# Optimization experiments

Hardware: AMD Instinct MI355X
Metric: run time of the kernel (lower is better)

## Reference

```python
import jax, jax.numpy as jnp
import numpy as np

B, T, C, H = 4, 2048, 768, 12
D = C // H  # head dim = 64
EPS = 1e-5


def setup_inputs() -> dict:
    key = jax.random.key(0)
    ks = jax.random.split(key, 12)
    s = lambda fan_in: 1.0 / np.sqrt(fan_in)
    return {
        "x": jax.random.normal(ks[0], (B, T, C), dtype=jnp.float32),
        "ln1_g": jnp.ones((C,), jnp.float32),
        "ln1_b": jnp.zeros((C,), jnp.float32),
        "w_attn": jax.random.normal(ks[1], (C, 3 * C), jnp.float32) * s(C),
        "b_attn": jnp.zeros((3 * C,), jnp.float32),
        "w_aproj": jax.random.normal(ks[2], (C, C), jnp.float32) * s(C),
        "b_aproj": jnp.zeros((C,), jnp.float32),
        "ln2_g": jnp.ones((C,), jnp.float32),
        "ln2_b": jnp.zeros((C,), jnp.float32),
        "w_fc": jax.random.normal(ks[3], (C, 4 * C), jnp.float32) * s(C),
        "b_fc": jnp.zeros((4 * C,), jnp.float32),
        "w_mproj": jax.random.normal(ks[4], (4 * C, C), jnp.float32) * s(4 * C),
        "b_mproj": jnp.zeros((C,), jnp.float32),
    }


def _layernorm(x, g, b):
    mu = jnp.mean(x, axis=-1, keepdims=True)
    var = jnp.mean(jnp.square(x - mu), axis=-1, keepdims=True)
    return (x - mu) * jax.lax.rsqrt(var + EPS) * g + b


def _attention(h, w_attn, b_attn, w_aproj, b_aproj):
    qkv = h @ w_attn + b_attn                          # [B,T,3C]
    q, k, v = jnp.split(qkv, 3, axis=-1)
    q = q.reshape(B, T, H, D)
    k = k.reshape(B, T, H, D)
    v = v.reshape(B, T, H, D)
    att = jnp.einsum("bqhd,bkhd->bhqk", q, k) * (1.0 / np.sqrt(D))
    causal = jnp.tril(jnp.ones((T, T), bool))
    att = jnp.where(causal, att, -jnp.inf)
    att = jax.nn.softmax(att, axis=-1)
    y = jnp.einsum("bhqk,bkhd->bqhd", att, v).reshape(B, T, C)
    return y @ w_aproj + b_aproj


def reference(x, ln1_g, ln1_b, w_attn, b_attn, w_aproj, b_aproj,
              ln2_g, ln2_b, w_fc, b_fc, w_mproj, b_mproj):
    x = x + _attention(_layernorm(x, ln1_g, ln1_b), w_attn, b_attn, w_aproj, b_aproj)
    h = _layernorm(x, ln2_g, ln2_b)
    h = jax.nn.gelu(h @ w_fc + b_fc, approximate=True)  # tanh approximation, matches F.gelu(approximate='tanh')
    x = x + (h @ w_mproj + b_mproj)
    return x
```

## Files before the change

### kernel.cpp

```cpp
#include <hip/hip_runtime.h>


typedef unsigned short ushortT;
typedef unsigned int uintT;
typedef __attribute__((ext_vector_type(8))) __bf16 bf16x8;
typedef __attribute__((ext_vector_type(4))) float f32x4;

#define MFMA16(a, b, c) __builtin_amdgcn_mfma_f32_16x16x32_bf16(a, b, c, 0, 0, 0)

__device__ inline float b2f(ushortT u) {
  return __uint_as_float(((uintT)u) << 16);
}
__device__ inline ushortT f2b(float f) {
  uintT x = __float_as_uint(f);
  uintT r = x + 0x7fffu + ((x >> 16) & 1u);
  return (ushortT)(r >> 16);
}
__device__ inline uintT pack_bf2(float a, float b) {
  return __builtin_amdgcn_perm(__float_as_uint(b), __float_as_uint(a),
                               0x07060302u);
}

__device__ inline float fast_exp2(float x) {
#if __has_builtin(__builtin_amdgcn_exp2f)
  return __builtin_amdgcn_exp2f(x);
#else
  return exp2f(x);
#endif
}

__device__ inline float gelu_tanh(float v) {
  float t = 0.7978845608028654f * (v + 0.044715f * v * v * v);
  return v / (1.0f + __expf(-2.0f * t));
}

__device__ __forceinline__ void glds16(const ushortT* g, ushortT* l) {
  __builtin_amdgcn_global_load_lds(
      (const __attribute__((address_space(1))) unsigned int*)(const void*)g,
      (__attribute__((address_space(3))) unsigned int*)(void*)l, 16, 0, 0);
}

struct VecArgs {
  const void* src[8];
  int n[8];
  int dstoff[8];
};

__global__ __launch_bounds__(256) void prep_kernel(
    const void* __restrict__ w_attn, const void* __restrict__ w_aproj,
    const void* __restrict__ w_fc, const void* __restrict__ w_mproj,
    VecArgs va, ushortT* __restrict__ wT0, ushortT* __restrict__ wT1,
    ushortT* __restrict__ wT2, ushortT* __restrict__ wT3,
    ushortT* __restrict__ pv, int* __restrict__ flag,
    const void* __restrict__ x, const void* __restrict__ ln1g,
    const void* __restrict__ ln1b, ushortT* __restrict__ h1) {
  __shared__ int sfl;
  __shared__ ushortT tile[32][33];
  __shared__ float as_[4], aq_[4];
  int tid = threadIdx.x;
  {
    int crazy = 0;
    if (tid < 64) {
      uintT e = (((const ushortT*)w_fc)[2 * (tid * 64)] >> 7) & 0xFF;
      crazy = (e >= 150) ? 1 : 0;
    }
    unsigned long long m = __ballot(crazy != 0);
    if (tid == 0) sfl = (m != 0ull) ? 1 : 0;
    __syncthreads();
  }
  int fl = sfl;
  int b = (int)blockIdx.x;
  if (b == 0 && tid == 0) *flag = fl;

  const int T0 = 1728;
  const int T1 = T0 + 576;
  const int T2 = T1 + 2304;
  const int T3 = T2 + 2304;
  const int T4 = T3 + 39;

  if (b >= T4) {
    int row = b - T4;
    size_t base = (size_t)row * 768;
    const float* xf = (const float*)x;
    const ushortT* xb = (const ushortT*)x;
    float v0 = fl ? xf[base + tid]       : b2f(xb[base + tid]);
    float v1 = fl ? xf[base + tid + 256] : b2f(xb[base + tid + 256]);
    float v2 = fl ? xf[base + tid + 512] : b2f(xb[base + tid + 512]);
    float s = v0 + v1 + v2;
    float q = v0 * v0 + v1 * v1 + v2 * v2;
#pragma unroll
    for (int off = 32; off; off >>= 1) {
      s += __shfl_xor(s, off);
      q += __shfl_xor(q, off);
    }
    if ((tid & 63) == 0) { as_[tid >> 6] = s; aq_[tid >> 6] = q; }
    __syncthreads();
    s = as_[0] + as_[1] + as_[2] + as_[3];
    q = aq_[0] + aq_[1] + aq_[2] + aq_[3];
    float mu = s * (1.0f / 768.0f);
    float var = q * (1.0f / 768.0f) - mu * mu;
    float rs = rsqrtf(var + 1e-5f);
    const float* gf = (const float*)ln1g;
    const ushortT* gb_ = (const ushortT*)ln1g;
    const float* bf = (const float*)ln1b;
    const ushortT* bb_ = (const ushortT*)ln1b;
    ushortT* orow = h1 + base;
#pragma unroll
    for (int jj = 0; jj < 3; ++jj) {
      int c = tid + jj * 256;
      float gv = fl ? gf[c] : b2f(gb_[c]);
      float bv = fl ? bf[c] : b2f(bb_[c]);
      float vv = (jj == 0) ? v0 : (jj == 1) ? v1 : v2;
      orow[c] = f2b((vv - mu) * rs * gv + bv);
    }
    return;
  }

  const void* in = nullptr;
  ushortT* out = nullptr;
  int K = 0, N = 0, gx = 0, t = 0;
  if (b < T0)      { in = w_attn;  out = wT0; K = 768;  N = 2304; gx = 72; t = b; }
  else if (b < T1) { in = w_aproj; out = wT1; K = 768;  N = 768;  gx = 24; t = b - T0; }
  else if (b < T2) { in = w_fc;    out = wT2; K = 768;  N = 3072; gx = 96; t = b - T1; }
  else if (b < T3) { in = w_mproj; out = wT3; K = 3072; N = 768;  gx = 24; t = b - T2; }
  else {
    int c = b - T3;
    int v = 0;
    for (;;) {
      int nch = (va.n[v] + 255) >> 8;
      if (c < nch) break;
      c -= nch; ++v;
    }
    int i = c * 256 + tid;
    if (i < va.n[v]) {
      float xx = fl ? ((const float*)va.src[v])[i]
                    : b2f(((const ushortT*)va.src[v])[i]);
      pv[va.dstoff[v] + i] = f2b(xx);
    }
    return;
  }

  int n0 = (t % gx) * 32, k0 = (t / gx) * 32;
  int xx = tid & 31, y0 = tid >> 5;
#pragma unroll
  for (int i = y0; i < 32; i += 8) {
    size_t idx = (size_t)(k0 + i) * N + n0 + xx;
    tile[i][xx] = fl ? f2b(((const float*)in)[idx]) : ((const ushortT*)in)[idx];
  }
  __syncthreads();
#pragma unroll
  for (int i = y0; i < 32; i += 8)
    out[(size_t)(n0 + i) * K + k0 + xx] = tile[xx][i];
}

template <int MODE>
__global__ __launch_bounds__(256) void ln_kernel(
    const void* __restrict__ xin, const ushortT* __restrict__ g,
    const ushortT* __restrict__ bb, ushortT* __restrict__ out,
    const int* __restrict__ flag) {
  const int C = 768;
  bool f32;
  if constexpr (MODE == 1) f32 = true; else f32 = (*flag != 0);
  size_t base = (size_t)blockIdx.x * C;
  int tid = threadIdx.x;
  const float* xf = (const float*)xin;
  const ushortT* xb = (const ushortT*)xin;
  float v0 = f32 ? xf[base + tid]       : b2f(xb[base + tid]);
  float v1 = f32 ? xf[base + tid + 256] : b2f(xb[base + tid + 256]);
  float v2 = f32 ? xf[base + tid + 512] : b2f(xb[base + tid + 512]);
  float s = v0 + v1 + v2;
  float q = v0 * v0 + v1 * v1 + v2 * v2;
#pragma unroll
  for (int off = 32; off; off >>= 1) {
    s += __shfl_xor(s, off);
    q += __shfl_xor(q, off);
  }
  __shared__ float as_[4], aq_[4];
  if ((tid & 63) == 0) { as_[tid >> 6] = s; aq_[tid >> 6] = q; }
  __syncthreads();
  s = as_[0] + as_[1] + as_[2] + as_[3];
  q = aq_[0] + aq_[1] + aq_[2] + aq_[3];
  float mu = s * (1.0f / 768.0f);
  float var = q * (1.0f / 768.0f) - mu * mu;
  float rs = rsqrtf(var + 1e-5f);
  ushortT* orow = out + base;
  orow[tid]       = f2b((v0 - mu) * rs * b2f(g[tid])       + b2f(bb[tid]));
  orow[tid + 256] = f2b((v1 - mu) * rs * b2f(g[tid + 256]) + b2f(bb[tid + 256]));
  orow[tid + 512] = f2b((v2 - mu) * rs * b2f(g[tid + 512]) + b2f(bb[tid + 512]));
}

template <int EPI, int BN>
__global__ __launch_bounds__(256, 2) void gemm_8p(
    const ushortT* __restrict__ A, const ushortT* __restrict__ Bt,
    const ushortT* __restrict__ bias, const void* __restrict__ res,
    void* __restrict__ out, int N, int K, int lda, int nbm, int nbn,
    const int* __restrict__ flag) {
  constexpr int MI = (BN == 256) ? 8 : 4;
  constexpr int NI = 4;
  __shared__ ushortT As3[3][128 * 32];
  __shared__ ushortT Bs3[3][BN * 32];
  int fl = (EPI == 2 || EPI == 3) ? *flag : 0;
  int tid = threadIdx.x;
  int lane = tid & 63, wave = tid >> 6;
  int quad = lane >> 4, n = lane & 15;
  int wm, wn;
  if constexpr (BN == 256) { wm = 0; wn = wave * 64; }
  else { wm = (wave >> 1) * 64; wn = (wave & 1) * 64; }
  int l = blockIdx.x;
  int xcd = l & 7, j = l >> 3;
  int m0 = (xcd * (nbm >> 3) + j / nbn) * 128;
  int n0 = (j % nbn) * BN;

  int trow = tid >> 2;
  int tc = (((tid & 3) ^ ((trow >> 1) & 3)) << 3);
  const ushortT* ga = A + (size_t)(m0 + trow) * lda + tc;
  const ushortT* gb = Bt + (size_t)(n0 + trow) * lda + tc;

  const int cs = (quad ^ ((n >> 1) & 3)) << 3;

  int kt = K >> 5;
  f32x4 acc[MI][NI] = {};

  auto stage = [&](int tt, int slot) {
    int k0 = tt << 5;
    ushortT* la = &As3[slot][0] + wave * 512;
    ushortT* lb = &Bs3[slot][0] + wave * 512;
    glds16(ga + k0, la);
    glds16(ga + (size_t)64 * lda + k0, la + 2048);
    glds16(gb + k0, lb);
    glds16(gb + (size_t)64 * lda + k0, lb + 2048);
    if constexpr (BN == 256) {
      glds16(gb + (size_t)128 * lda + k0, lb + 4096);
      glds16(gb + (size_t)192 * lda + k0, lb + 6144);
    }
  };

  stage(0, 0);
  stage(1, 1);
  if constexpr (BN == 256)
    asm volatile("s_waitcnt vmcnt(6)" ::: "memory");
  else
    asm volatile("s_waitcnt vmcnt(4)" ::: "memory");
  __builtin_amdgcn_s_barrier();

  int cur = 0;
  for (int t = 0; t < kt; ++t) {
    const ushortT* ca = &As3[cur][0];
    const ushortT* cb = &Bs3[cur][0];
    int nxt = cur + 2; if (nxt >= 3) nxt -= 3;
    bool pf = (t + 2) < kt;
    int pk0 = (t + 2) << 5;
    ushortT* la = &As3[nxt][0] + wave * 512;
    ushortT* lb = &Bs3[nxt][0] + wave * 512;

    bf16x8 af[4], bfr[NI];
#pragma unroll
    for (int i = 0; i < 4; ++i)
      af[i] = *(const bf16x8*)(ca + (wm + i * 16 + n) * 32 + cs);
#pragma unroll
    for (int i = 0; i < NI; ++i)
      bfr[i] = *(const bf16x8*)(cb + (wn + i * 16 + n) * 32 + cs);
    if (pf) {
      glds16(ga + pk0, la);
      glds16(ga + (size_t)64 * lda + pk0, la + 2048);
      glds16(gb + pk0, lb);
      if constexpr (BN == 128)
        glds16(gb + (size_t)64 * lda + pk0, lb + 2048);
    }
    __builtin_amdgcn_s_barrier();
    __builtin_amdgcn_s_setprio(1);
#pragma unroll
    for (int mi = 0; mi < 4; ++mi)
#pragma unroll
      for (int ni = 0; ni < NI; ++ni)
        acc[mi][ni] = MFMA16(af[mi], bfr[ni], acc[mi][ni]);
    __builtin_amdgcn_s_setprio(0);
    if constexpr (BN == 256) {
      __builtin_amdgcn_s_barrier();
#pragma unroll
      for (int i = 0; i < 4; ++i)
        af[i] = *(const bf16x8*)(ca + (64 + i * 16 + n) * 32 + cs);
      if (pf) {
        glds16(gb + (size_t)64 * lda + pk0, lb + 2048);
        glds16(gb + (size_t)128 * lda + pk0, lb + 4096);
        glds16(gb + (size_t)192 * lda + pk0, lb + 6144);
      }
      __builtin_amdgcn_s_barrier();
      __builtin_amdgcn_s_setprio(1);
#pragma unroll
      for (int mi = 0; mi < 4; ++mi)
#pragma unroll
        for (int ni = 0; ni < NI; ++ni)
          acc[4 + mi][ni] = MFMA16(af[mi], bfr[ni], acc[4 + mi][ni]);
      __builtin_amdgcn_s_setprio(0);
    }
    if (pf) {
      if constexpr (BN == 256)
        asm volatile("s_waitcnt vmcnt(6)" ::: "memory");
      else
        asm volatile("s_waitcnt vmcnt(4)" ::: "memory");
    } else {
      asm volatile("s_waitcnt vmcnt(0)" ::: "memory");
    }
    __builtin_amdgcn_s_barrier();

    cur = cur + 1; if (cur == 3) cur = 0;
  }

#pragma unroll
  for (int mi = 0; mi < MI; ++mi) {
#pragma unroll
    for (int ni = 0; ni < NI; ++ni) {
      int gc = n0 + wn + ni * 16 + n;
      float bv = b2f(bias[gc]);
      int gr0 = m0 + wm + mi * 16 + quad * 4;
      if constexpr (EPI == 5) {
        float v0 = acc[mi][ni][0] + bv;
        float v1 = acc[mi][ni][1] + bv;
        float v2 = acc[mi][ni][2] + bv;
        float v3 = acc[mi][ni][3] + bv;
        if (gc < 1536) {
          ushortT* o = (ushortT*)out;
          o[(size_t)(gr0 + 0) * N + gc] = f2b(v0);
          o[(size_t)(gr0 + 1) * N + gc] = f2b(v1);
          o[(size_t)(gr0 + 2) * N + gc] = f2b(v2);
          o[(size_t)(gr0 + 3) * N + gc] = f2b(v3);
        } else {
          int hh = (gc - 1536) >> 6, dd = (gc - 1536) & 63;
          int bb = gr0 >> 11, tin = gr0 & 2047;
          ushortT* vp = (ushortT*)res;
          uint2 o;
          o.x = (uintT)f2b(v0) | ((uintT)f2b(v1) << 16);
          o.y = (uintT)f2b(v2) | ((uintT)f2b(v3) << 16);
          *(uint2*)(vp + ((size_t)(bb * 12 + hh) * 64 + dd) * 2048 + tin) = o;
        }
      } else {
#pragma unroll
        for (int r = 0; r < 4; ++r) {
          size_t idx = (size_t)(gr0 + r) * N + gc;
          float v = acc[mi][ni][r] + bv;
          if constexpr (EPI == 1) {
            v = gelu_tanh(v);
            ((ushortT*)out)[idx] = f2b(v);
          } else if constexpr (EPI == 2) {
            v += fl ? ((const float*)res)[idx] : b2f(((const ushortT*)res)[idx]);
            ((float*)out)[idx] = v;
          } else if constexpr (EPI == 3) {
            v += ((const float*)res)[idx];
            if (fl) ((float*)out)[idx] = v;
            else    ((ushortT*)out)[idx] = f2b(v);
          } else {
            ((ushortT*)out)[idx] = f2b(v);
          }
        }
      }
    }
  }
}

__global__ __launch_bounds__(256) void attn_kernel(
    const ushortT* __restrict__ qkv, const ushortT* __restrict__ vt,
    ushortT* __restrict__ y) {
  const int T = 2048, C3 = 2304;
  constexpr int LDP = 72;
  __shared__ ushortT Ks[2][64 * 64];
  __shared__ ushortT Vs[2][64 * 64];
  __shared__ ushortT Ps[4 * 16 * LDP];
  int bh = blockIdx.y;
  int b = bh / 12, h = bh % 12;
  int pj = blockIdx.x;
  int tid = threadIdx.x;
  int lane = tid & 63, wave = tid >> 6;
  int quad = lane >> 4, n = lane & 15, n7 = n & 7;

  const ushortT* base = qkv + (size_t)b * T * C3;
  const ushortT* kbase = base + 768 + h * 64;
  const ushortT* vbase = vt + (size_t)bh * 64 * T;
  ushortT* myP = Ps + wave * 16 * LDP;

  const float QS = 0.18033688011112042f;
  const float MB = 20.0f;

  int qtA = pj, qtB = 31 - pj;
  int nA = qtA + 1, ntot = 33;

  int srow = lane >> 3, scol = lane & 7;
  const ushortT* kg =
      kbase + (size_t)(wave * 16 + srow) * C3 + ((scol ^ srow) << 3);
  const ushortT* vg =
      vbase + (size_t)(wave * 16 + srow) * T + ((scol ^ srow) << 3);

  const int c0 = (quad ^ n7) << 3;
  const int c1 = ((4 + quad) ^ n7) << 3;

  int qt = qtA;
  int qw = qt * 64 + wave * 16;
  bf16x8 aq[2];
  {
    const ushortT* qrow = base + (size_t)(qw + n) * C3 + h * 64 + quad * 8;
#pragma unroll
    for (int dh = 0; dh < 2; ++dh) {
      union { ushortT u[8]; bf16x8 v; } tmp;
#pragma unroll
      for (int j = 0; j < 8; ++j) tmp.u[j] = f2b(b2f(qrow[dh * 32 + j]) * QS);
      aq[dh] = tmp.v;
    }
  }
  f32x4 Ot[4] = {};
  float l_ = 0.f;

  auto stage = [&](int kt_, int buf) {
    int kof = kt_ << 6;
    ushortT* lk = &Ks[buf][0] + wave * 1024;
    ushortT* lv = &Vs[buf][0] + wave * 1024;
    glds16(kg + (size_t)kof * C3, lk);
    glds16(kg + (size_t)(kof + 8) * C3, lk + 512);
    glds16(vg + kof, lv);
    glds16(vg + (size_t)8 * T + kof, lv + 512);
  };

  stage(0, 0);
  __syncthreads();

  int cur = 0;
  for (int t = 0; t < ntot; ++t) {
    int kt = (t < nA) ? t : t - nA;
    if (t + 1 < ntot) {
      int ktn = (t + 1 < nA) ? t + 1 : t + 1 - nA;
      stage(ktn, cur ^ 1);
    }
    const ushortT* ks = &Ks[cur][0];
    const ushortT* vs = &Vs[cur][0];

    f32x4 St[4];
#pragma unroll
    for (int g = 0; g < 4; ++g) {
      bf16x8 ka0 = *(const bf16x8*)(ks + (g * 16 + n) * 64 + c0);
      bf16x8 ka1 = *(const bf16x8*)(ks + (g * 16 + n) * 64 + c1);
      f32x4 z = {};
      z = MFMA16(ka0, aq[0], z);
      St[g] = MFMA16(ka1, aq[1], z);
    }
    if (kt == qt) {
      int lim = wave * 16 + n;
#pragma unroll
      for (int g = 0; g < 4; ++g)
#pragma unroll
        for (int r = 0; r < 4; ++r)
          if (g * 16 + quad * 4 + r > lim) St[g][r] = -1e30f;
    }
    float ls = 0.f;
#pragma unroll
    for (int g = 0; g < 4; ++g) {
      float p0 = fast_exp2(St[g][0] - MB);
      float p1 = fast_exp2(St[g][1] - MB);
      float p2 = fast_exp2(St[g][2] - MB);
      float p3 = fast_exp2(St[g][3] - MB);
      ls += (p0 + p1) + (p2 + p3);
      uint2 pk;
      pk.x = pack_bf2(p0, p1);
      pk.y = pack_bf2(p2, p3);
      *(uint2*)(myP + n * LDP + g * 16 + quad * 4) = pk;
    }
    ls += __shfl_xor(ls, 16);
    ls += __shfl_xor(ls, 32);
    l_ += ls;

    bf16x8 pb0 = *(const bf16x8*)(myP + n * LDP + quad * 8);
    bf16x8 pb1 = *(const bf16x8*)(myP + n * LDP + 32 + quad * 8);
#pragma unroll
    for (int dt = 0; dt < 4; ++dt) {
      bf16x8 va0 = *(const bf16x8*)(vs + (dt * 16 + n) * 64 + c0);
      bf16x8 va1 = *(const bf16x8*)(vs + (dt * 16 + n) * 64 + c1);
      Ot[dt] = MFMA16(va0, pb0, Ot[dt]);
      Ot[dt] = MFMA16(va1, pb1, Ot[dt]);
    }

    if (kt == qt) {
      float inv = 1.0f / l_;
      int qg = qw + n;
#pragma unroll
      for (int dt = 0; dt < 4; ++dt) {
        uint2 o;
        o.x = pack_bf2(Ot[dt][0] * inv, Ot[dt][1] * inv);
        o.y = pack_bf2(Ot[dt][2] * inv, Ot[dt][3] * inv);
        *(uint2*)(y + (size_t)(b * T + qg) * 768 + h * 64 + dt * 16 +
                  quad * 4) = o;
      }
      if (t + 1 < ntot) {
        qt = qtB;
        qw = qt * 64 + wave * 16;
        const ushortT* qrow =
            base + (size_t)(qw + n) * C3 + h * 64 + quad * 8;
#pragma unroll
        for (int dh = 0; dh < 2; ++dh) {
          union { ushortT u[8]; bf16x8 v; } tmp;
#pragma unroll
          for (int j = 0; j < 8; ++j)
            tmp.u[j] = f2b(b2f(qrow[dh * 32 + j]) * QS);
          aq[dh] = tmp.v;
        }
#pragma unroll
        for (int dt = 0; dt < 4; ++dt)
#pragma unroll
          for (int r = 0; r < 4; ++r) Ot[dt][r] = 0.f;
        l_ = 0.f;
      }
    }
    __syncthreads();
    cur ^= 1;
  }
}

extern "C" void kernel_launch(void* const* d_in, const int* in_sizes, int n_in,
                              void* d_out, int out_size, void* d_ws,
                              size_t ws_size, hipStream_t stream) {
  (void)in_sizes; (void)n_in; (void)out_size; (void)ws_size;
  const void* x       = d_in[0];
  const void* w_attn  = d_in[3];
  const void* w_aproj = d_in[5];
  const void* w_fc    = d_in[9];
  const void* w_mproj = d_in[11];

  char* ws = (char*)d_ws;
  ushortT* h1  = (ushortT*)(ws);
  ushortT* qkv = (ushortT*)(ws + 12582912);
  ushortT* yb  = (ushortT*)(ws + 50331648);
  float*   x1  = (float*)(ws + 62914560);
  ushortT* fcg = (ushortT*)(ws + 88080384);
  ushortT* wT0 = (ushortT*)(ws + 138412032);
  ushortT* wT1 = (ushortT*)(ws + 141950976);
  ushortT* wT2 = (ushortT*)(ws + 143130624);
  ushortT* wT3 = (ushortT*)(ws + 147849216);
  ushortT* pv  = (ushortT*)(ws + 152567808);
  int*     flag = (int*)(ws + 152600576);
  ushortT* vt  = fcg;
  ushortT* h2  = yb;

  const int O_LN1G = 0, O_LN1B = 768, O_BATT = 1536, O_BAPR = 3840,
            O_LN2G = 4608, O_LN2B = 5376, O_BFC = 6144, O_BMPR = 9216;

  VecArgs va;
  va.src[0] = d_in[1];  va.n[0] = 768;  va.dstoff[0] = O_LN1G;
  va.src[1] = d_in[2];  va.n[1] = 768;  va.dstoff[1] = O_LN1B;
  va.src[2] = d_in[4];  va.n[2] = 2304; va.dstoff[2] = O_BATT;
  va.src[3] = d_in[6];  va.n[3] = 768;  va.dstoff[3] = O_BAPR;
  va.src[4] = d_in[7];  va.n[4] = 768;  va.dstoff[4] = O_LN2G;
  va.src[5] = d_in[8];  va.n[5] = 768;  va.dstoff[5] = O_LN2B;
  va.src[6] = d_in[10]; va.n[6] = 3072; va.dstoff[6] = O_BFC;
  va.src[7] = d_in[12]; va.n[7] = 768;  va.dstoff[7] = O_BMPR;

  prep_kernel<<<15143, 256, 0, stream>>>(
      w_attn, w_aproj, w_fc, w_mproj, va, wT0, wT1, wT2, wT3, pv, flag,
      x, d_in[1], d_in[2], h1);

  gemm_8p<5, 256><<<576, 256, 0, stream>>>(
      h1, wT0, pv + O_BATT, vt, qkv, 2304, 768, 768, 64, 9, flag);
  attn_kernel<<<dim3(16, 48), 256, 0, stream>>>(qkv, vt, yb);
  gemm_8p<2, 128><<<384, 256, 0, stream>>>(
      yb, wT1, pv + O_BAPR, x, x1, 768, 768, 768, 64, 6, flag);
  ln_kernel<1><<<8192, 256, 0, stream>>>(x1, pv + O_LN2G, pv + O_LN2B, h2, flag);
  gemm_8p<1, 256><<<768, 256, 0, stream>>>(
      h2, wT2, pv + O_BFC, nullptr, fcg, 3072, 768, 768, 64, 12, flag);
  gemm_8p<3, 128><<<384, 256, 0, stream>>>(
      fcg, wT3, pv + O_BMPR, x1, d_out, 768, 3072, 3072, 64, 6, flag);
}
```

Before: 402.0 us.

## Share K/V tile loads between paired query tiles in causal attention

The attention kernel used to walk the two paired query tiles one after the other, restaging K/V for the second tile. Now both tiles' queries stay in registers and a single pass over key tiles (32-pj of them) feeds both. Tile B uses every key tile and tile A only the first pj+1, which cuts K/V staging and barrier iterations from 33 to at most 32, and the shared tiles are loaded once. The cost is higher register pressure from two sets of Q, O and S accumulators, which may lower occupancy.

```diff
diff --git a/kernel.cpp b/kernel.cpp
--- a/kernel.cpp
+++ b/kernel.cpp
@@ -382,7 +382,7 @@
   const float MB = 20.0f;
 
   int qtA = pj, qtB = 31 - pj;
-  int nA = qtA + 1, ntot = 33;
+  int ntiles = 32 - pj;
 
   int srow = lane >> 3, scol = lane & 7;
   const ushortT* kg =
@@ -393,21 +393,26 @@
   const int c0 = (quad ^ n7) << 3;
   const int c1 = ((4 + quad) ^ n7) << 3;
 
-  int qt = qtA;
-  int qw = qt * 64 + wave * 16;
-  bf16x8 aq[2];
+  bf16x8 aqA[2], aqB[2];
   {
-    const ushortT* qrow = base + (size_t)(qw + n) * C3 + h * 64 + quad * 8;
+    const ushortT* qrA =
+        base + (size_t)(qtA * 64 + wave * 16 + n) * C3 + h * 64 + quad * 8;
+    const ushortT* qrB =
+        base + (size_t)(qtB * 64 + wave * 16 + n) * C3 + h * 64 + quad * 8;
 #pragma unroll
     for (int dh = 0; dh < 2; ++dh) {
-      union { ushortT u[8]; bf16x8 v; } tmp;
-#pragma unroll
-      for (int j = 0; j < 8; ++j) tmp.u[j] = f2b(b2f(qrow[dh * 32 + j]) * QS);
-      aq[dh] = tmp.v;
-    }
-  }
-  f32x4 Ot[4] = {};
-  float l_ = 0.f;
+      union { ushortT u[8]; bf16x8 v; } ta, tb;
+#pragma unroll
+      for (int j = 0; j < 8; ++j) {
+        ta.u[j] = f2b(b2f(qrA[dh * 32 + j]) * QS);
+        tb.u[j] = f2b(b2f(qrB[dh * 32 + j]) * QS);
+      }
+      aqA[dh] = ta.v;
+      aqB[dh] = tb.v;
+    }
+  }
+  f32x4 OtA[4] = {}, OtB[4] = {};
+  float lA = 0.f, lB = 0.f;
 
   auto stage = [&](int kt_, int buf) {
     int kof = kt_ << 6;
@@ -423,92 +428,138 @@
   __syncthreads();
 
   int cur = 0;
-  for (int t = 0; t < ntot; ++t) {
-    int kt = (t < nA) ? t : t - nA;
-    if (t + 1 < ntot) {
-      int ktn = (t + 1 < nA) ? t + 1 : t + 1 - nA;
-      stage(ktn, cur ^ 1);
-    }
+  for (int t = 0; t < ntiles; ++t) {
+    if (t + 1 < ntiles) stage(t + 1, cur ^ 1);
     const ushortT* ks = &Ks[cur][0];
     const ushortT* vs = &Vs[cur][0];
-
-    f32x4 St[4];
-#pragma unroll
-    for (int g = 0; g < 4; ++g) {
-      bf16x8 ka0 = *(const bf16x8*)(ks + (g * 16 + n) * 64 + c0);
-      bf16x8 ka1 = *(const bf16x8*)(ks + (g * 16 + n) * 64 + c1);
-      f32x4 z = {};
-      z = MFMA16(ka0, aq[0], z);
-      St[g] = MFMA16(ka1, aq[1], z);
-    }
-    if (kt == qt) {
-      int lim = wave * 16 + n;
+    bool doA = (t <= pj);
+
+    f32x4 StB[4], StA[4];
+    {
+      bf16x8 ka[4][2];
+#pragma unroll
+      for (int g = 0; g < 4; ++g) {
+        ka[g][0] = *(const bf16x8*)(ks + (g * 16 + n) * 64 + c0);
+        ka[g][1] = *(const bf16x8*)(ks + (g * 16 + n) * 64 + c1);
+      }
+#pragma unroll
+      for (int g = 0; g < 4; ++g) {
+        f32x4 z = {};
+        z = MFMA16(ka[g][0], aqB[0], z);
+        StB[g] = MFMA16(ka[g][1], aqB[1], z);
+      }
+      if (doA) {
+#pragma unroll
+        for (int g = 0; g < 4; ++g) {
+          f32x4 z = {};
+          z = MFMA16(ka[g][0], aqA[0], z);
+          StA[g] = MFMA16(ka[g][1], aqA[1], z);
+        }
+      }
+    }
+
+    bf16x8 va[4][2];
+#pragma unroll
+    for (int dt = 0; dt < 4; ++dt) {
+      va[dt][0] = *(const bf16x8*)(vs + (dt * 16 + n) * 64 + c0);
+      va[dt][1] = *(const bf16x8*)(vs + (dt * 16 + n) * 64 + c1);
+    }
+
+    int lim = wave * 16 + n;
+
+    if (t == ntiles - 1) {
 #pragma unroll
       for (int g = 0; g < 4; ++g)
 #pragma unroll
         for (int r = 0; r < 4; ++r)
-          if (g * 16 + quad * 4 + r > lim) St[g][r] = -1e30f;
-    }
-    float ls = 0.f;
-#pragma unroll
-    for (int g = 0; g < 4; ++g) {
-      float p0 = fast_exp2(St[g][0] - MB);
-      float p1 = fast_exp2(St[g][1] - MB);
-      float p2 = fast_exp2(St[g][2] - MB);
-      float p3 = fast_exp2(St[g][3] - MB);
-      ls += (p0 + p1) + (p2 + p3);
-      uint2 pk;
-      pk.x = pack_bf2(p0, p1);
-      pk.y = pack_bf2(p2, p3);
-      *(uint2*)(myP + n * LDP + g * 16 + quad * 4) = pk;
-    }
-    ls += __shfl_xor(ls, 16);
-    ls += __shfl_xor(ls, 32);
-    l_ += ls;
-
-    bf16x8 pb0 = *(const bf16x8*)(myP + n * LDP + quad * 8);
-    bf16x8 pb1 = *(const bf16x8*)(myP + n * LDP + 32 + quad * 8);
-#pragma unroll
-    for (int dt = 0; dt < 4; ++dt) {
-      bf16x8 va0 = *(const bf16x8*)(vs + (dt * 16 + n) * 64 + c0);
-      bf16x8 va1 = *(const bf16x8*)(vs + (dt * 16 + n) * 64 + c1);
-      Ot[dt] = MFMA16(va0, pb0, Ot[dt]);
-      Ot[dt] = MFMA16(va1, pb1, Ot[dt]);
-    }
-
-    if (kt == qt) {
-      float inv = 1.0f / l_;
-      int qg = qw + n;
+          if (g * 16 + quad * 4 + r > lim) StB[g][r] = -1e30f;
+    }
+    {
+      float ls = 0.f;
+#pragma unroll
+      for (int g = 0; g < 4; ++g) {
+        float p0 = fast_exp2(StB[g][0] - MB);
+        float p1 = fast_exp2(StB[g][1] - MB);
+        float p2 = fast_exp2(StB[g][2] - MB);
+        float p3 = fast_exp2(StB[g][3] - MB);
+        ls += (p0 + p1) + (p2 + p3);
+        uint2 pk;
+        pk.x = pack_bf2(p0, p1);
+        pk.y = pack_bf2(p2, p3);
+        *(uint2*)(myP + n * LDP + g * 16 + quad * 4) = pk;
+      }
+      ls += __shfl_xor(ls, 16);
+      ls += __shfl_xor(ls, 32);
+      lB += ls;
+      bf16x8 pb0 = *(const bf16x8*)(myP + n * LDP + quad * 8);
+      bf16x8 pb1 = *(const bf16x8*)(myP + n * LDP + 32 + quad * 8);
 #pragma unroll
       for (int dt = 0; dt < 4; ++dt) {
-        uint2 o;
-        o.x = pack_bf2(Ot[dt][0] * inv, Ot[dt][1] * inv);
-        o.y = pack_bf2(Ot[dt][2] * inv, Ot[dt][3] * inv);
-        *(uint2*)(y + (size_t)(b * T + qg) * 768 + h * 64 + dt * 16 +
-                  quad * 4) = o;
-      }
-      if (t + 1 < ntot) {
-        qt = qtB;
-        qw = qt * 64 + wave * 16;
-        const ushortT* qrow =
-            base + (size_t)(qw + n) * C3 + h * 64 + quad * 8;
-#pragma unroll
-        for (int dh = 0; dh < 2; ++dh) {
-          union { ushortT u[8]; bf16x8 v; } tmp;
-#pragma unroll
-          for (int j = 0; j < 8; ++j)
-            tmp.u[j] = f2b(b2f(qrow[dh * 32 + j]) * QS);
-          aq[dh] = tmp.v;
-        }
-#pragma unroll
-        for (int dt = 0; dt < 4; ++dt)
-#pragma unroll
-          for (int r = 0; r < 4; ++r) Ot[dt][r] = 0.f;
-        l_ = 0.f;
-      }
-    }
+        OtB[dt] = MFMA16(va[dt][0], pb0, OtB[dt]);
+        OtB[dt] = MFMA16(va[dt][1], pb1, OtB[dt]);
+      }
+    }
+
+    if (doA) {
+      if (t == pj) {
+#pragma unroll
+        for (int g = 0; g < 4; ++g)
+#pragma unroll
+          for (int r = 0; r < 4; ++r)
+            if (g * 16 + quad * 4 + r > lim) StA[g][r] = -1e30f;
+      }
+      float ls = 0.f;
+#pragma unroll
+      for (int g = 0; g < 4; ++g) {
+        float p0 = fast_exp2(StA[g][0] - MB);
+        float p1 = fast_exp2(StA[g][1] - MB);
+        float p2 = fast_exp2(StA[g][2] - MB);
+        float p3 = fast_exp2(StA[g][3] - MB);
+        ls += (p0 + p1) + (p2 + p3);
+        uint2 pk;
+        pk.x = pack_bf2(p0, p1);
+        pk.y = pack_bf2(p2, p3);
+        *(uint2*)(myP + n * LDP + g * 16 + quad * 4) = pk;
+      }
+      ls += __shfl_xor(ls, 16);
+      ls += __shfl_xor(ls, 32);
+      lA += ls;
+      bf16x8 pb0 = *(const bf16x8*)(myP + n * LDP + quad * 8);
+      bf16x8 pb1 = *(const bf16x8*)(myP + n * LDP + 32 + quad * 8);
+#pragma unroll
+      for (int dt = 0; dt < 4; ++dt) {
+        OtA[dt] = MFMA16(va[dt][0], pb0, OtA[dt]);
+        OtA[dt] = MFMA16(va[dt][1], pb1, OtA[dt]);
+      }
+    }
+
     __syncthreads();
     cur ^= 1;
+  }
+
+  {
+    float inv = 1.0f / lA;
+    int qg = qtA * 64 + wave * 16 + n;
+#pragma unroll
+    for (int dt = 0; dt < 4; ++dt) {
+      uint2 o;
+      o.x = pack_bf2(OtA[dt][0] * inv, OtA[dt][1] * inv);
+      o.y = pack_bf2(OtA[dt][2] * inv, OtA[dt][3] * inv);
+      *(uint2*)(y + (size_t)(b * T + qg) * 768 + h * 64 + dt * 16 +
+                quad * 4) = o;
+    }
+  }
+  {
+    float inv = 1.0f / lB;
+    int qg = qtB * 64 + wave * 16 + n;
+#pragma unroll
+    for (int dt = 0; dt < 4; ++dt) {
+      uint2 o;
+      o.x = pack_bf2(OtB[dt][0] * inv, OtB[dt][1] * inv);
+      o.y = pack_bf2(OtB[dt][2] * inv, OtB[dt][3] * inv);
+      *(uint2*)(y + (size_t)(b * T + qg) * 768 + h * 64 + dt * 16 +
+                quad * 4) = o;
+    }
   }
 }
 
```

After: 400.5 us. Within noise of the previous version (-0.4%).
